# Optimization experiments

Measured on AMD Instinct MI355X. Metric: run time of the kernel, lower is better.

Reference implementation:

```python
import jax, jax.numpy as jnp
import numpy as np

N = 4096   # nodes
E = 4096   # hyperedges (== N so the original's [N,H] output is fully populated)
F = 256    # feature_size
H = 256    # hidden_size
BLOCK = 64 # node-block size for the blocked masked max/min scan


def setup_inputs() -> dict:
    key = jax.random.key(0)
    ks = jax.random.split(key, 11)
    mask = jax.random.randint(ks[4], (E, N), 0, 2, dtype=jnp.int32)
    # guarantee every hyperedge is non-empty (matches `if end > start` path)
    mask = mask.at[jnp.arange(E), jnp.arange(N)].set(1)
    s = 0.05
    return {
        "pos_features": jax.random.normal(ks[0], (N, F), jnp.float32),
        "pos_matrix": jax.random.normal(ks[1], (N, F), jnp.float32),
        "neg_features": jax.random.normal(ks[2], (N, F), jnp.float32),
        "neg_matrix": jax.random.normal(ks[3], (N, F), jnp.float32),
        "batch_mask": mask,
        "W_self": jax.random.normal(ks[5], (F, H), jnp.float32) * s,
        "b_self": jnp.zeros((H,), jnp.float32),
        "W_hyper": jax.random.normal(ks[6], (F, H), jnp.float32) * s,
        "b_hyper": jnp.zeros((H,), jnp.float32),
        "W_score": jax.random.normal(ks[7], (H, 1), jnp.float32) * s,
        "b_score": jnp.zeros((1,), jnp.float32),
    }


def maxmin_pool(mask_bool, feats):
    """Per-hyperedge (max - min) over member-node features.
    mask_bool: [E, N] bool, feats: [N, H] -> [E, H].
    Blocked over nodes to avoid materializing [E, N, H]."""
    Ee, Nn = mask_bool.shape
    Hh = feats.shape[1]
    nb = Nn // BLOCK
    mask_blocks = mask_bool.reshape(Ee, nb, BLOCK).transpose(1, 0, 2)  # [nb, E, BLOCK]
    feat_blocks = feats.reshape(nb, BLOCK, Hh)                          # [nb, BLOCK, H]

    def body(carry, xs):
        mx, mn = carry
        mblk, fblk = xs                      # [E, BLOCK], [BLOCK, H]
        m = mblk[:, :, None]                 # [E, BLOCK, 1]
        f = fblk[None]                       # [1, BLOCK, H]
        mx = jnp.maximum(mx, jnp.max(jnp.where(m, f, -jnp.inf), axis=1))
        mn = jnp.minimum(mn, jnp.min(jnp.where(m, f, jnp.inf), axis=1))
        return (mx, mn), None

    init = (jnp.full((Ee, Hh), -jnp.inf, feats.dtype),
            jnp.full((Ee, Hh), jnp.inf, feats.dtype))
    (mx, mn), _ = jax.lax.scan(body, init, (mask_blocks, feat_blocks))
    return mx - mn


def reference(pos_features, pos_matrix, neg_features, neg_matrix, batch_mask,
              W_self, b_self, W_hyper, b_hyper, W_score, b_score):
    mask = batch_mask.astype(bool)

    def branch(x_feat, x_mat):
        h = jax.nn.relu(x_feat @ W_self + b_self + x_mat @ W_hyper + b_hyper)  # [N, H]
        pooled = maxmin_pool(mask, h)                                          # [E, H]
        return jax.nn.sigmoid(pooled @ W_score + b_score)                      # [E, 1]

    pos_score = branch(pos_features, pos_matrix)
    neg_score = branch(neg_features, neg_matrix)
    return pos_score, neg_score
```

## Files before the change

kernel.cpp:

```cpp
#include <hip/hip_runtime.h>
#include <hip/hip_bf16.h>
#include <hip/hip_fp16.h>


typedef short bf16x8 __attribute__((ext_vector_type(8)));
typedef float f32x4 __attribute__((ext_vector_type(4)));
typedef short s16x2 __attribute__((ext_vector_type(2)));
typedef unsigned short u16x2 __attribute__((ext_vector_type(2)));

static __device__ __forceinline__ unsigned short f2bf(float f) {
    __hip_bfloat16 b = __float2bfloat16(f);
    return __builtin_bit_cast(unsigned short, b);
}
static __device__ __forceinline__ float f16u_to_f(unsigned u) {
    __half h = __builtin_bit_cast(__half, (unsigned short)(u & 0xffffu));
    return __half2float(h);
}
static __device__ __forceinline__ unsigned pkmax_i16(unsigned a, unsigned b) {
    s16x2 r = __builtin_elementwise_max(__builtin_bit_cast(s16x2, a), __builtin_bit_cast(s16x2, b));
    return __builtin_bit_cast(unsigned, r);
}
static __device__ __forceinline__ unsigned pkmin_u16(unsigned a, unsigned b) {
    u16x2 r = __builtin_elementwise_min(__builtin_bit_cast(u16x2, a), __builtin_bit_cast(u16x2, b));
    return __builtin_bit_cast(unsigned, r);
}

__global__ void k_prep(const int* __restrict__ mask, unsigned* __restrict__ packed,
                       const float* __restrict__ Ws, const float* __restrict__ Wh,
                       unsigned short* __restrict__ Wts, unsigned short* __restrict__ Wth) {
    const int bx = blockIdx.x, t = threadIdx.x;
    if (bx < 2048) {
        int w = bx * 256 + t;
        const int* p = mask + (size_t)w * 32;
        unsigned word = 0;
#pragma unroll
        for (int j = 0; j < 32; j += 4) {
            int4 m = *(const int4*)(p + j);
            word |= (m.x != 0 ? (1u << (31 - j)) : 0u)
                  | (m.y != 0 ? (1u << (30 - j)) : 0u)
                  | (m.z != 0 ? (1u << (29 - j)) : 0u)
                  | (m.w != 0 ? (1u << (28 - j)) : 0u);
        }
        packed[w] = word;
    } else {
        int b2 = bx - 2048;
        int k = b2 & 255, brn = b2 >> 8;
        const float* W     = brn ? Wh : Ws;
        unsigned short* Wt = brn ? Wth : Wts;
        Wt[t * 256 + k] = f2bf(W[k * 256 + t]);
    }
}

__launch_bounds__(256)
__global__ void k_gemm_relu(const float* __restrict__ pXf, const float* __restrict__ pXm,
                            const float* __restrict__ nXf, const float* __restrict__ nXm,
                            const unsigned short* __restrict__ Wts, const unsigned short* __restrict__ Wth,
                            const float* __restrict__ bs,  const float* __restrict__ bh,
                            unsigned short* __restrict__ hAll ) {
    const int t  = threadIdx.x;
    const int wv = t >> 6;
    const int l  = t & 63;
    const int lm = l & 15;
    const int q  = l >> 4;
    const int bz = blockIdx.z;
    const float* Xf = bz ? nXf : pXf;
    const float* Xm = bz ? nXm : pXm;
    unsigned short* hb = hAll + (size_t)bz * 4096 * 256;

    const int m0 = blockIdx.x * 64 + wv * 16;
    const int n0 = blockIdx.y * 64;

    f32x4 acc[4] = {};
#pragma unroll
    for (int ks = 0; ks < 512; ks += 32) {
        const float* X           = (ks < 256) ? Xf : Xm;
        const unsigned short* Wt = (ks < 256) ? Wts : Wth;
        const int kk = (ks & 255) + q * 8;
        float4 a0 = *(const float4*)(X + (m0 + lm) * 256 + kk);
        float4 a1 = *(const float4*)(X + (m0 + lm) * 256 + kk + 4);
        bf16x8 a;
        a[0] = (short)f2bf(a0.x); a[1] = (short)f2bf(a0.y);
        a[2] = (short)f2bf(a0.z); a[3] = (short)f2bf(a0.w);
        a[4] = (short)f2bf(a1.x); a[5] = (short)f2bf(a1.y);
        a[6] = (short)f2bf(a1.z); a[7] = (short)f2bf(a1.w);
#pragma unroll
        for (int nt = 0; nt < 4; nt++) {
            bf16x8 b = *(const bf16x8*)(Wt + (n0 + nt * 16 + lm) * 256 + kk);
            acc[nt] = __builtin_amdgcn_mfma_f32_16x16x32_bf16(a, b, acc[nt], 0, 0, 0);
        }
    }
#pragma unroll
    for (int nt = 0; nt < 4; nt++) {
        const int c = n0 + nt * 16 + lm;
        const float bsum = bs[c] + bh[c];
#pragma unroll
        for (int i = 0; i < 4; i++) {
            const int r = m0 + q * 4 + i;
            float v = acc[nt][i] + bsum;
            v = v > 0.f ? v : 0.f;
            hb[r * 256 + c] = __builtin_bit_cast(unsigned short, __float2half(v));
        }
    }
}

__global__ void k_transposeH(const unsigned short* __restrict__ h, unsigned short* __restrict__ hT) {
    __shared__ unsigned tile[64][65];
    const int r0 = blockIdx.x * 64, c0 = blockIdx.y * 64, br = blockIdx.z;
    const unsigned short* src = h + (size_t)br * 4096 * 256;
    unsigned short* dst = hT + (size_t)br * 256 * 4096;
    const int t = threadIdx.x;
#pragma unroll
    for (int m = 0; m < 16; m++) {
        int li = t + m * 256; int r = li >> 6, c = li & 63;
        tile[r][c] = src[(size_t)(r0 + r) * 256 + c0 + c];
    }
    __syncthreads();
#pragma unroll
    for (int m = 0; m < 16; m++) {
        int li = t + m * 256; int c = li >> 6, r = li & 63;
        dst[(size_t)(c0 + c) * 4096 + r0 + r] = (unsigned short)tile[r][c];
    }
}

__launch_bounds__(256)
__global__ void k_sort(const unsigned short* __restrict__ hT,
                       unsigned* __restrict__ sortedAsc,
                       unsigned* __restrict__ topkG, unsigned* __restrict__ botkG) {
    __shared__ unsigned arrA[4096];
    __shared__ unsigned arrB[4096];
    __shared__ unsigned short hist[16 * 256];

    const int c = blockIdx.x, br = blockIdx.y, t = threadIdx.x;
    const int wv = t >> 6, l = t & 63;
    const unsigned short* src = hT + (size_t)(br * 256 + c) * 4096;

    {
        uint4 a = ((const uint4*)src)[t * 2];
        uint4 b = ((const uint4*)src)[t * 2 + 1];
        unsigned base = t * 16;
        unsigned w[8] = {a.x, a.y, a.z, a.w, b.x, b.y, b.z, b.w};
#pragma unroll
        for (int m = 0; m < 8; m++) {
            arrA[base + 2 * m]     = ((w[m] & 0xFFFFu) << 16) | (base + 2 * m);
            arrA[base + 2 * m + 1] = (w[m] & 0xFFFF0000u)     | (base + 2 * m + 1);
        }
    }
    __syncthreads();

    unsigned* A = arrA;
    unsigned* B = arrB;
#pragma unroll
    for (int pass = 0; pass < 4; pass++) {
        const int sh = 16 + pass * 4;
        unsigned keys[16];
        unsigned short cnt[16];
#pragma unroll
        for (int b = 0; b < 16; b++) cnt[b] = 0;
#pragma unroll
        for (int m = 0; m < 16; m++) {
            keys[m] = A[t * 16 + m];
            cnt[(keys[m] >> sh) & 15u]++;
        }
#pragma unroll
        for (int b = 0; b < 16; b++) hist[b * 256 + t] = cnt[b];
        __syncthreads();

        unsigned loc[16];
        unsigned sum = 0;
#pragma unroll
        for (int m = 0; m < 16; m++) { loc[m] = sum; sum += hist[t * 16 + m]; }
        unsigned ws = sum;
#pragma unroll
        for (int off = 1; off < 64; off <<= 1) {
            unsigned n = __shfl_up(ws, off);
            if (l >= off) ws += n;
        }
        if (l == 63) B[wv] = ws;
        __syncthreads();
        unsigned wbase = 0;
#pragma unroll
        for (int w2 = 0; w2 < 4; w2++) if (w2 < wv) wbase += B[w2];
        const unsigned ex = wbase + ws - sum;
#pragma unroll
        for (int m = 0; m < 16; m++) hist[t * 16 + m] = (unsigned short)(ex + loc[m]);
        __syncthreads();

        unsigned offs[16];
#pragma unroll
        for (int b = 0; b < 16; b++) offs[b] = hist[b * 256 + t];
#pragma unroll
        for (int m = 0; m < 16; m++) {
            unsigned b = (keys[m] >> sh) & 15u;
            B[offs[b]++] = keys[m];
        }
        __syncthreads();
        unsigned* tmp = A; A = B; B = tmp;
    }

    unsigned* outp = sortedAsc + (size_t)(br * 256 + c) * 4096;
#pragma unroll
    for (int m = 0; m < 16; m++) { int i = t + m * 256; outp[i] = arrA[i]; }
    if (t < 16) {
        topkG[(br * 16 + t) * 256 + c] = arrA[4095 - t];
        botkG[(br * 16 + t) * 256 + c] = arrA[t];
    }
}

__launch_bounds__(256)
__global__ void k_probe(const unsigned* __restrict__ sortedAsc,
                        const unsigned* __restrict__ topkG,
                        const unsigned* __restrict__ botkG,
                        const unsigned* __restrict__ packed,
                        const float* __restrict__ Wscore,
                        const float* __restrict__ bscore,
                        float* __restrict__ out) {
    __shared__ __align__(16) unsigned topkL[16 * 256];
    __shared__ __align__(16) unsigned botkL[16 * 256];
    __shared__ __align__(16) unsigned bitsL[16 * 128];

    const int t  = threadIdx.x;
    const int wv = t >> 6;
    const int l  = t & 63;
    const int e0 = blockIdx.x * 16;
    const int br = blockIdx.y;

    {
        const uint4* ts  = (const uint4*)(topkG + br * 4096);
        const uint4* bs2 = (const uint4*)(botkG + br * 4096);
#pragma unroll
        for (int m = 0; m < 4; m++) {
            ((uint4*)topkL)[t + m * 256] = ts[t + m * 256];
            ((uint4*)botkL)[t + m * 256] = bs2[t + m * 256];
        }
        ((uint4*)bitsL)[t]       = ((const uint4*)(packed + e0 * 128))[t];
        ((uint4*)bitsL)[t + 256] = ((const uint4*)(packed + e0 * 128))[t + 256];
    }
    __syncthreads();

    const float bsc = *bscore;
    float wsv[4];
#pragma unroll
    for (int sl = 0; sl < 4; sl++) wsv[sl] = Wscore[l + 64 * sl];

#pragma unroll 1
    for (int k = 0; k < 4; k++) {
        const int e = wv * 4 + k;
        const unsigned* mk = &bitsL[e * 128];
        float s = 0.f;
#pragma unroll
        for (int sl = 0; sl < 4; sl++) {
            const int c = l + 64 * sl;
            const unsigned* gs = sortedAsc + (size_t)(br * 256 + c) * 4096;

            unsigned sel = 0xFFFFFFFFu;
#pragma unroll 1
            for (int g = 0; g < 2; g++) {
                unsigned kk[8]; int ss[8];
#pragma unroll
                for (int j = 0; j < 8; j++) kk[j] = topkL[(g * 8 + j) * 256 + c];
#pragma unroll
                for (int j = 0; j < 8; j++)
                    ss[j] = (int)(mk[(kk[j] & 4095u) >> 5] << (kk[j] & 31u));
                unsigned fnd = 0xFFFFFFFFu;
#pragma unroll
                for (int j = 7; j >= 0; j--) if (ss[j] < 0) fnd = kk[j];
                if (fnd != 0xFFFFFFFFu) { sel = fnd; break; }
            }
            if (sel == 0xFFFFFFFFu) {
#pragma unroll 1
                for (int p = 16; p < 4096; p++) {
                    unsigned key = gs[4095 - p];
                    if ((int)(mk[(key & 4095u) >> 5] << (key & 31u)) < 0) { sel = key; break; }
                }
            }
            const float vmax = f16u_to_f(sel >> 16);

            sel = 0xFFFFFFFFu;
#pragma unroll 1
            for (int g = 0; g < 2; g++) {
                unsigned kk[8]; int ss[8];
#pragma unroll
                for (int j = 0; j < 8; j++) kk[j] = botkL[(g * 8 + j) * 256 + c];
#pragma unroll
                for (int j = 0; j < 8; j++)
                    ss[j] = (int)(mk[(kk[j] & 4095u) >> 5] << (kk[j] & 31u));
                unsigned fnd = 0xFFFFFFFFu;
#pragma unroll
                for (int j = 7; j >= 0; j--) if (ss[j] < 0) fnd = kk[j];
                if (fnd != 0xFFFFFFFFu) { sel = fnd; break; }
            }
            if (sel == 0xFFFFFFFFu) {
#pragma unroll 1
                for (int p = 16; p < 4096; p++) {
                    unsigned key = gs[p];
                    if ((int)(mk[(key & 4095u) >> 5] << (key & 31u)) < 0) { sel = key; break; }
                }
            }
            const float vmin = f16u_to_f(sel >> 16);

            s += (vmax - vmin) * wsv[sl];
        }
#pragma unroll
        for (int off = 32; off; off >>= 1) s += __shfl_xor(s, off);
        if (l == 0)
            out[br * 4096 + e0 + e] = 1.f / (1.f + __expf(-(s + bsc)));
    }
}

#define POOL_STEP(WE, MX0, MX1, MN0, MN1, VX, VY)                          \
    {                                                                      \
        asm("s_add_u32 %[we], %[we], %[we]\n\t"                            \
            "s_cbranch_scc0 Lskip%=\n\t"                                   \
            "v_pk_max_i16 %[mx0], %[mx0], %[vx]\n\t"                       \
            "v_pk_max_i16 %[mx1], %[mx1], %[vy]\n\t"                       \
            "v_pk_min_u16 %[mn0], %[mn0], %[vx]\n\t"                       \
            "v_pk_min_u16 %[mn1], %[mn1], %[vy]\n"                         \
            "Lskip%=:"                                                     \
            : [we] "+s"(WE),                                               \
              [mx0] "+v"(MX0), [mx1] "+v"(MX1),                            \
              [mn0] "+v"(MN0), [mn1] "+v"(MN1)                             \
            : [vx] "v"(VX), [vy] "v"(VY)                                   \
            : "scc");                                                      \
    }

__launch_bounds__(512, 8)
__global__ void k_pool9(const unsigned short* __restrict__ hAll,
                        const unsigned* __restrict__ packed,
                        const float* __restrict__ Wscore,
                        const float* __restrict__ bscore,
                        float* __restrict__ out) {
    __shared__ __align__(16) unsigned bits[4 * 128];
    __shared__ __align__(16) unsigned part[8][4][64][4];

    const int t  = threadIdx.x;
    const int wv = t >> 6;
    const int l  = t & 63;
    const int e0 = blockIdx.x * 4;
    const int br = blockIdx.y;
    const unsigned short* h = hAll + (size_t)br * 4096 * 256;

    if (t < 128) ((uint4*)bits)[t] = ((const uint4*)(packed + e0 * 128))[t];
    __syncthreads();

    unsigned mx0[4], mx1[4], mn0[4], mn1[4];
#pragma unroll
    for (int e = 0; e < 4; e++) {
        mx0[e] = 0x80008000u; mx1[e] = 0x80008000u;
        mn0[e] = 0xFFFFFFFFu; mn1[e] = 0xFFFFFFFFu;
    }

#pragma unroll 1
    for (int ch = 0; ch < 16; ch++) {
        const int w0 = wv * 16 + ch;
        unsigned we0 = (unsigned)__builtin_amdgcn_readfirstlane((int)bits[0 * 128 + w0]);
        unsigned we1 = (unsigned)__builtin_amdgcn_readfirstlane((int)bits[1 * 128 + w0]);
        unsigned we2 = (unsigned)__builtin_amdgcn_readfirstlane((int)bits[2 * 128 + w0]);
        unsigned we3 = (unsigned)__builtin_amdgcn_readfirstlane((int)bits[3 * 128 + w0]);

        const unsigned short* hp = h + (size_t)(wv * 512 + ch * 32) * 256 + 4 * l;
#pragma unroll
        for (int jj = 0; jj < 8; jj++) {
            uint2 v0 = *(const uint2*)(hp + (jj * 4 + 0) * 256);
            uint2 v1 = *(const uint2*)(hp + (jj * 4 + 1) * 256);
            uint2 v2 = *(const uint2*)(hp + (jj * 4 + 2) * 256);
            uint2 v3 = *(const uint2*)(hp + (jj * 4 + 3) * 256);

            POOL_STEP(we0, mx0[0], mx1[0], mn0[0], mn1[0], v0.x, v0.y);
            POOL_STEP(we1, mx0[1], mx1[1], mn0[1], mn1[1], v0.x, v0.y);
            POOL_STEP(we2, mx0[2], mx1[2], mn0[2], mn1[2], v0.x, v0.y);
            POOL_STEP(we3, mx0[3], mx1[3], mn0[3], mn1[3], v0.x, v0.y);
            POOL_STEP(we0, mx0[0], mx1[0], mn0[0], mn1[0], v1.x, v1.y);
            POOL_STEP(we1, mx0[1], mx1[1], mn0[1], mn1[1], v1.x, v1.y);
            POOL_STEP(we2, mx0[2], mx1[2], mn0[2], mn1[2], v1.x, v1.y);
            POOL_STEP(we3, mx0[3], mx1[3], mn0[3], mn1[3], v1.x, v1.y);
            POOL_STEP(we0, mx0[0], mx1[0], mn0[0], mn1[0], v2.x, v2.y);
            POOL_STEP(we1, mx0[1], mx1[1], mn0[1], mn1[1], v2.x, v2.y);
            POOL_STEP(we2, mx0[2], mx1[2], mn0[2], mn1[2], v2.x, v2.y);
            POOL_STEP(we3, mx0[3], mx1[3], mn0[3], mn1[3], v2.x, v2.y);
            POOL_STEP(we0, mx0[0], mx1[0], mn0[0], mn1[0], v3.x, v3.y);
            POOL_STEP(we1, mx0[1], mx1[1], mn0[1], mn1[1], v3.x, v3.y);
            POOL_STEP(we2, mx0[2], mx1[2], mn0[2], mn1[2], v3.x, v3.y);
            POOL_STEP(we3, mx0[3], mx1[3], mn0[3], mn1[3], v3.x, v3.y);
        }
    }

#pragma unroll
    for (int e = 0; e < 4; e++) {
        uint4 p; p.x = mx0[e]; p.y = mx1[e]; p.z = mn0[e]; p.w = mn1[e];
        *(uint4*)&part[wv][e][l][0] = p;
    }
    __syncthreads();

    if (wv < 4) {
        unsigned rmx0 = 0x80008000u, rmx1 = 0x80008000u;
        unsigned rmn0 = 0xFFFFFFFFu, rmn1 = 0xFFFFFFFFu;
#pragma unroll
        for (int w2 = 0; w2 < 8; w2++) {
            uint4 p = *(const uint4*)&part[w2][wv][l][0];
            rmx0 = pkmax_i16(rmx0, p.x);  rmx1 = pkmax_i16(rmx1, p.y);
            rmn0 = pkmin_u16(rmn0, p.z);  rmn1 = pkmin_u16(rmn1, p.w);
        }
        float4 wsv = *(const float4*)(Wscore + 4 * l);
        const float bsc = *bscore;
        float s = (f16u_to_f(rmx0)       - f16u_to_f(rmn0))       * wsv.x
                + (f16u_to_f(rmx0 >> 16) - f16u_to_f(rmn0 >> 16)) * wsv.y
                + (f16u_to_f(rmx1)       - f16u_to_f(rmn1))       * wsv.z
                + (f16u_to_f(rmx1 >> 16) - f16u_to_f(rmn1 >> 16)) * wsv.w;
#pragma unroll
        for (int off = 32; off; off >>= 1) s += __shfl_xor(s, off);
        if (l == 0)
            out[br * 4096 + e0 + wv] = 1.f / (1.f + __expf(-(s + bsc)));
    }
}

extern "C" void kernel_launch(void* const* d_in, const int* in_sizes, int n_in,
                              void* d_out, int out_size, void* d_ws, size_t ws_size,
                              hipStream_t stream) {
    const float* pf  = (const float*)d_in[0];
    const float* pm  = (const float*)d_in[1];
    const float* nf  = (const float*)d_in[2];
    const float* nm  = (const float*)d_in[3];
    const int*   msk = (const int*)d_in[4];
    const float* Wsf = (const float*)d_in[5];
    const float* bsf = (const float*)d_in[6];
    const float* Whp = (const float*)d_in[7];
    const float* bhp = (const float*)d_in[8];
    const float* Wsc = (const float*)d_in[9];
    const float* bsc = (const float*)d_in[10];
    float* out = (float*)d_out;

    char* ws = (char*)d_ws;
    const size_t MB = 1024u * 1024u;
    unsigned short* hbuf  = (unsigned short*)(ws);
    unsigned short* hT    = (unsigned short*)(ws + 4 * MB);
    unsigned*       srt   = (unsigned*)(ws + 8 * MB);
    unsigned*       pck   = (unsigned*)(ws + 16 * MB);
    unsigned short* Wts   = (unsigned short*)(ws + 18 * MB);
    unsigned short* Wth   = Wts + 256 * 256;
    unsigned*       topkG = (unsigned*)(ws + 18 * MB + 256 * 1024);
    unsigned*       botkG = (unsigned*)(ws + 18 * MB + 256 * 1024 + 32768);
    const size_t need = 18 * MB + 256 * 1024 + 2 * 32768;

    k_prep<<<2560, 256, 0, stream>>>(msk, pck, Wsf, Whp, Wts, Wth);
    k_gemm_relu<<<dim3(64, 4, 2), 256, 0, stream>>>(pf, pm, nf, nm, Wts, Wth, bsf, bhp, hbuf);

    if (ws_size >= need) {
        k_transposeH<<<dim3(64, 4, 2), 256, 0, stream>>>(hbuf, hT);
        k_sort<<<dim3(256, 2), 256, 0, stream>>>(hT, srt, topkG, botkG);
        k_probe<<<dim3(256, 2), 256, 0, stream>>>(srt, topkG, botkG, pck, Wsc, bsc, out);
    } else {
        k_pool9<<<dim3(1024, 2), 512, 0, stream>>>(hbuf, pck, Wsc, bsc, out);
    }
}
```

Measured before the change: 190.6 us.

## Write GEMM output transposed, drop full sorted array, keep top/bottom-64

The GEMM epilogue now writes h directly in column-major (transposed) layout with vectorized stores, which removes the separate transpose kernel. The sort kernel no longer writes the full 4096-entry sorted key array per column and instead keeps the top and bottom 64 keys. The probe kernel falls back to those 64-entry lists and, if no masked member is found there, to a direct masked scan of the transposed column. This cuts one launch and about 8 MB of global writes and reads. The cost is a slower rare fallback path and a probe kernel that needs to look at the reference code again.

```diff
diff --git a/kernel.cpp b/kernel.cpp
--- a/kernel.cpp
+++ b/kernel.cpp
@@ -56,7 +56,7 @@
                             const float* __restrict__ nXf, const float* __restrict__ nXm,
                             const unsigned short* __restrict__ Wts, const unsigned short* __restrict__ Wth,
                             const float* __restrict__ bs,  const float* __restrict__ bh,
-                            unsigned short* __restrict__ hAll ) {
+                            unsigned short* __restrict__ hOut, int tmode) {
     const int t  = threadIdx.x;
     const int wv = t >> 6;
     const int l  = t & 63;
@@ -65,7 +65,7 @@
     const int bz = blockIdx.z;
     const float* Xf = bz ? nXf : pXf;
     const float* Xm = bz ? nXm : pXm;
-    unsigned short* hb = hAll + (size_t)bz * 4096 * 256;
+    unsigned short* hb = hOut + (size_t)bz * 4096 * 256;
 
     const int m0 = blockIdx.x * 64 + wv * 16;
     const int n0 = blockIdx.y * 64;
@@ -89,42 +89,38 @@
             acc[nt] = __builtin_amdgcn_mfma_f32_16x16x32_bf16(a, b, acc[nt], 0, 0, 0);
         }
     }
-#pragma unroll
-    for (int nt = 0; nt < 4; nt++) {
-        const int c = n0 + nt * 16 + lm;
-        const float bsum = bs[c] + bh[c];
-#pragma unroll
-        for (int i = 0; i < 4; i++) {
-            const int r = m0 + q * 4 + i;
-            float v = acc[nt][i] + bsum;
-            v = v > 0.f ? v : 0.f;
-            hb[r * 256 + c] = __builtin_bit_cast(unsigned short, __float2half(v));
-        }
-    }
-}
-
-__global__ void k_transposeH(const unsigned short* __restrict__ h, unsigned short* __restrict__ hT) {
-    __shared__ unsigned tile[64][65];
-    const int r0 = blockIdx.x * 64, c0 = blockIdx.y * 64, br = blockIdx.z;
-    const unsigned short* src = h + (size_t)br * 4096 * 256;
-    unsigned short* dst = hT + (size_t)br * 256 * 4096;
-    const int t = threadIdx.x;
-#pragma unroll
-    for (int m = 0; m < 16; m++) {
-        int li = t + m * 256; int r = li >> 6, c = li & 63;
-        tile[r][c] = src[(size_t)(r0 + r) * 256 + c0 + c];
-    }
-    __syncthreads();
-#pragma unroll
-    for (int m = 0; m < 16; m++) {
-        int li = t + m * 256; int c = li >> 6, r = li & 63;
-        dst[(size_t)(c0 + c) * 4096 + r0 + r] = (unsigned short)tile[r][c];
+    if (tmode) {
+#pragma unroll
+        for (int nt = 0; nt < 4; nt++) {
+            const int c = n0 + nt * 16 + lm;
+            const float bsum = bs[c] + bh[c];
+            ushort4 v4;
+#pragma unroll
+            for (int i = 0; i < 4; i++) {
+                float v = acc[nt][i] + bsum;
+                v = v > 0.f ? v : 0.f;
+                ((unsigned short*)&v4)[i] = __builtin_bit_cast(unsigned short, __float2half(v));
+            }
+            *(ushort4*)(hb + (size_t)c * 4096 + m0 + q * 4) = v4;
+        }
+    } else {
+#pragma unroll
+        for (int nt = 0; nt < 4; nt++) {
+            const int c = n0 + nt * 16 + lm;
+            const float bsum = bs[c] + bh[c];
+#pragma unroll
+            for (int i = 0; i < 4; i++) {
+                const int r = m0 + q * 4 + i;
+                float v = acc[nt][i] + bsum;
+                v = v > 0.f ? v : 0.f;
+                hb[(size_t)r * 256 + c] = __builtin_bit_cast(unsigned short, __float2half(v));
+            }
+        }
     }
 }
 
 __launch_bounds__(256)
 __global__ void k_sort(const unsigned short* __restrict__ hT,
-                       unsigned* __restrict__ sortedAsc,
                        unsigned* __restrict__ topkG, unsigned* __restrict__ botkG) {
     __shared__ unsigned arrA[4096];
     __shared__ unsigned arrB[4096];
@@ -197,20 +193,17 @@
         unsigned* tmp = A; A = B; B = tmp;
     }
 
-    unsigned* outp = sortedAsc + (size_t)(br * 256 + c) * 4096;
-#pragma unroll
-    for (int m = 0; m < 16; m++) { int i = t + m * 256; outp[i] = arrA[i]; }
-    if (t < 16) {
-        topkG[(br * 16 + t) * 256 + c] = arrA[4095 - t];
-        botkG[(br * 16 + t) * 256 + c] = arrA[t];
+    if (t < 64) {
+        topkG[(br * 64 + t) * 256 + c] = arrA[4095 - t];
+        botkG[(br * 64 + t) * 256 + c] = arrA[t];
     }
 }
 
 __launch_bounds__(256)
-__global__ void k_probe(const unsigned* __restrict__ sortedAsc,
-                        const unsigned* __restrict__ topkG,
+__global__ void k_probe(const unsigned* __restrict__ topkG,
                         const unsigned* __restrict__ botkG,
                         const unsigned* __restrict__ packed,
+                        const unsigned short* __restrict__ hT,
                         const float* __restrict__ Wscore,
                         const float* __restrict__ bscore,
                         float* __restrict__ out) {
@@ -225,8 +218,8 @@
     const int br = blockIdx.y;
 
     {
-        const uint4* ts  = (const uint4*)(topkG + br * 4096);
-        const uint4* bs2 = (const uint4*)(botkG + br * 4096);
+        const uint4* ts  = (const uint4*)(topkG + br * 16384);
+        const uint4* bs2 = (const uint4*)(botkG + br * 16384);
 #pragma unroll
         for (int m = 0; m < 4; m++) {
             ((uint4*)topkL)[t + m * 256] = ts[t + m * 256];
@@ -250,7 +243,6 @@
 #pragma unroll
         for (int sl = 0; sl < 4; sl++) {
             const int c = l + 64 * sl;
-            const unsigned* gs = sortedAsc + (size_t)(br * 256 + c) * 4096;
 
             unsigned sel = 0xFFFFFFFFu;
 #pragma unroll 1
@@ -267,11 +259,20 @@
                 if (fnd != 0xFFFFFFFFu) { sel = fnd; break; }
             }
             if (sel == 0xFFFFFFFFu) {
-#pragma unroll 1
-                for (int p = 16; p < 4096; p++) {
-                    unsigned key = gs[4095 - p];
+                const unsigned* tg = topkG + br * 16384 + c;
+#pragma unroll 1
+                for (int p = 16; p < 64; p++) {
+                    unsigned key = tg[p * 256];
                     if ((int)(mk[(key & 4095u) >> 5] << (key & 31u)) < 0) { sel = key; break; }
                 }
+            }
+            if (sel == 0xFFFFFFFFu) {
+                const unsigned short* col = hT + (size_t)(br * 256 + c) * 4096;
+                unsigned best = 0;
+#pragma unroll 1
+                for (int n = 0; n < 4096; n++)
+                    if ((int)(mk[n >> 5] << (n & 31)) < 0) { unsigned v = col[n]; if (v > best) best = v; }
+                sel = best << 16;
             }
             const float vmax = f16u_to_f(sel >> 16);
 
@@ -290,11 +291,20 @@
                 if (fnd != 0xFFFFFFFFu) { sel = fnd; break; }
             }
             if (sel == 0xFFFFFFFFu) {
-#pragma unroll 1
-                for (int p = 16; p < 4096; p++) {
-                    unsigned key = gs[p];
+                const unsigned* bg = botkG + br * 16384 + c;
+#pragma unroll 1
+                for (int p = 16; p < 64; p++) {
+                    unsigned key = bg[p * 256];
                     if ((int)(mk[(key & 4095u) >> 5] << (key & 31u)) < 0) { sel = key; break; }
                 }
+            }
+            if (sel == 0xFFFFFFFFu) {
+                const unsigned short* col = hT + (size_t)(br * 256 + c) * 4096;
+                unsigned best = 0xFFFFu;
+#pragma unroll 1
+                for (int n = 0; n < 4096; n++)
+                    if ((int)(mk[n >> 5] << (n & 31)) < 0) { unsigned v = col[n]; if (v < best) best = v; }
+                sel = best << 16;
             }
             const float vmin = f16u_to_f(sel >> 16);
 
@@ -432,23 +442,21 @@
     char* ws = (char*)d_ws;
     const size_t MB = 1024u * 1024u;
     unsigned short* hbuf  = (unsigned short*)(ws);
-    unsigned short* hT    = (unsigned short*)(ws + 4 * MB);
-    unsigned*       srt   = (unsigned*)(ws + 8 * MB);
-    unsigned*       pck   = (unsigned*)(ws + 16 * MB);
-    unsigned short* Wts   = (unsigned short*)(ws + 18 * MB);
+    unsigned*       pck   = (unsigned*)(ws + 4 * MB);
+    unsigned short* Wts   = (unsigned short*)(ws + 6 * MB);
     unsigned short* Wth   = Wts + 256 * 256;
-    unsigned*       topkG = (unsigned*)(ws + 18 * MB + 256 * 1024);
-    unsigned*       botkG = (unsigned*)(ws + 18 * MB + 256 * 1024 + 32768);
-    const size_t need = 18 * MB + 256 * 1024 + 2 * 32768;
+    unsigned*       topkG = (unsigned*)(ws + 6 * MB + 256 * 1024);
+    unsigned*       botkG = (unsigned*)(ws + 6 * MB + 384 * 1024);
+    const size_t need = 6 * MB + 512 * 1024;
 
     k_prep<<<2560, 256, 0, stream>>>(msk, pck, Wsf, Whp, Wts, Wth);
-    k_gemm_relu<<<dim3(64, 4, 2), 256, 0, stream>>>(pf, pm, nf, nm, Wts, Wth, bsf, bhp, hbuf);
 
     if (ws_size >= need) {
-        k_transposeH<<<dim3(64, 4, 2), 256, 0, stream>>>(hbuf, hT);
-        k_sort<<<dim3(256, 2), 256, 0, stream>>>(hT, srt, topkG, botkG);
-        k_probe<<<dim3(256, 2), 256, 0, stream>>>(srt, topkG, botkG, pck, Wsc, bsc, out);
+        k_gemm_relu<<<dim3(64, 4, 2), 256, 0, stream>>>(pf, pm, nf, nm, Wts, Wth, bsf, bhp, hbuf, 1);
+        k_sort<<<dim3(256, 2), 256, 0, stream>>>(hbuf, topkG, botkG);
+        k_probe<<<dim3(256, 2), 256, 0, stream>>>(topkG, botkG, pck, hbuf, Wsc, bsc, out);
     } else {
+        k_gemm_relu<<<dim3(64, 4, 2), 256, 0, stream>>>(pf, pm, nf, nm, Wts, Wth, bsf, bhp, hbuf, 0);
         k_pool9<<<dim3(1024, 2), 512, 0, stream>>>(hbuf, pck, Wsc, bsc, out);
     }
 }
```

After: 189.6 us. No clear change (-0.5%).
